# Kernel tuning notes

Hardware: AMD Instinct MI355X
Metric: run time of the kernel (lower is better)

The kernel has to match this reference:

```python
import jax, jax.numpy as jnp
import numpy as np

L = 262144
C = 64           # in_channels == out_channels (required by zeros_like scatter)
NUM_MODES = 64

def setup_inputs() -> dict:
    key = jax.random.key(0)
    k1, k2, k3, k4 = jax.random.split(key, 4)
    u = jax.random.normal(k1, (L, C), dtype=jnp.float32)
    y = jax.random.uniform(k2, (1, 1), dtype=jnp.float32)
    scale = 1.0 / (C * C)
    K = scale * jax.random.normal(k3, (2, C, C, NUM_MODES), dtype=jnp.float32)
    # glorot_normal for square (C, C)
    W = jax.random.normal(k4, (C, C), dtype=jnp.float32) * jnp.sqrt(2.0 / (C + C))
    return {"u": u, "y": y, "K": K, "W": W}

def reference(u, y, K, W):
    num_modes = K.shape[-1]
    out_ch = W.shape[0]
    # conditioner: spectral (global) branch
    u_hat = jnp.fft.rfft(u, axis=0)                      # (L//2+1, C) complex64
    Kc = K[0] + 1j * K[1]                                # (C, C, num_modes)
    z_modes = jnp.einsum('xi,iox->xo', u_hat[:num_modes], Kc)  # (num_modes, C)
    z_global = jnp.zeros_like(u_hat).at[:num_modes, :].set(z_modes)
    # conditioner: local branch (gather one spatial row, apply W)
    length = u.shape[0]
    idx = jnp.int32(y * length)[0][0]
    z_local = jnp.dot(W, u[idx, :out_ch])                # (C,)
    # basefield: inverse transform + local shift
    n = 2 * (z_global.shape[0] - 1)                      # == L
    s = jnp.fft.irfft(z_global, n=n, axis=0)             # (L, C)
    return s + z_local
```

## Files before the change

### kernel.cpp

```cpp
#include <hip/hip_runtime.h>

#define LN 262144
#define LMASK 262143
#define NCH 64
#define INV_L (1.0f/262144.0f)
#define BSTR 38
#define ISTR 138
#define XSTR 66

typedef short short8 __attribute__((ext_vector_type(8)));
typedef float f32x4 __attribute__((ext_vector_type(4)));

static __device__ __forceinline__ unsigned short f2bf(float x) {
    union { float f; unsigned u; } v; v.f = x;
    unsigned r = (v.u + 0x7fff + ((v.u >> 16) & 1)) >> 16;
    return (unsigned short)r;
}
static __device__ __forceinline__ float fsin01(float rev) {
    float r; asm("v_sin_f32 %0, %1" : "=v"(r) : "v"(rev)); return r;
}
static __device__ __forceinline__ float fcos01(float rev) {
    float r; asm("v_cos_f32 %0, %1" : "=v"(r) : "v"(rev)); return r;
}

__global__ __launch_bounds__(256) void fno_fwd(const float* __restrict__ u,
                                               float* __restrict__ part, int nb) {
    __shared__ __align__(16) unsigned short Bt[2][64 * BSTR];
    const int tid = threadIdx.x;
    const int lane = tid & 63;
    const int w = tid >> 6;
    const int chunk = LN / nb;
    const int ksteps = chunk >> 5;
    const int n0 = blockIdx.x * chunk;

    const int kkst = tid >> 3;
    const int gst = tid & 7;

    const int l15 = lane & 15;
    const int hk = lane >> 4;
    const int m = w * 16 + l15;

    float cR[8], sR[8];
    #pragma unroll
    for (int j = 0; j < 8; ++j) {
        int ph = (m * (n0 + hk * 8 + j)) & LMASK;
        cR[j] = fcos01((float)ph * INV_L);
        sR[j] = fsin01((float)ph * INV_L);
    }
    float cD, sD;
    {
        int ph = (m * 32) & LMASK;
        cD = fcos01((float)ph * INV_L);
        sD = fsin01((float)ph * INV_L);
    }

    f32x4 accC[4], accS[4];
    #pragma unroll
    for (int t = 0; t < 4; ++t) { accC[t] = (f32x4){0,0,0,0}; accS[t] = (f32x4){0,0,0,0}; }

    const float* __restrict__ ub = u + (size_t)(n0 + kkst) * NCH + gst * 8;
    const size_t tstep = 32 * NCH;

    float4 a0 = *(const float4*)(ub);
    float4 a1 = *(const float4*)(ub + 4);
    float4 b0 = *(const float4*)(ub + tstep);
    float4 b1 = *(const float4*)(ub + tstep + 4);
    {
        float uv[8] = {a0.x, a0.y, a0.z, a0.w, a1.x, a1.y, a1.z, a1.w};
        #pragma unroll
        for (int q = 0; q < 8; ++q)
            Bt[0][(gst * 8 + q) * BSTR + kkst] = f2bf(uv[q]);
    }
    a0 = b0; a1 = b1;
    b0 = *(const float4*)(ub + 2 * tstep);
    b1 = *(const float4*)(ub + 2 * tstep + 4);

    for (int t = 0; t < ksteps; ++t) {
        __syncthreads();
        if (t + 1 < ksteps) {
            float uv[8] = {a0.x, a0.y, a0.z, a0.w, a1.x, a1.y, a1.z, a1.w};
            unsigned short* bt = Bt[(t + 1) & 1];
            #pragma unroll
            for (int q = 0; q < 8; ++q)
                bt[(gst * 8 + q) * BSTR + kkst] = f2bf(uv[q]);
        }
        a0 = b0; a1 = b1;
        if (t + 3 < ksteps) {
            const float* pn = ub + (size_t)(t + 3) * tstep;
            b0 = *(const float4*)(pn);
            b1 = *(const float4*)(pn + 4);
        }
        short8 aC, aS;
        #pragma unroll
        for (int j = 0; j < 8; ++j) {
            aC[j] = (short)f2bf(cR[j]);
            aS[j] = (short)f2bf(-sR[j]);
        }
        #pragma unroll
        for (int j = 0; j < 8; ++j) {
            float c2 = cR[j] * cD - sR[j] * sD;
            sR[j] = fmaf(sR[j], cD, cR[j] * sD);
            cR[j] = c2;
        }
        const unsigned short* bt = Bt[t & 1];
        #pragma unroll
        for (int tn = 0; tn < 4; ++tn) {
            const short8 bf = *(const short8*)&bt[(tn * 16 + l15) * BSTR + hk * 8];
            accC[tn] = __builtin_amdgcn_mfma_f32_16x16x32_bf16(aC, bf, accC[tn], 0, 0, 0);
            accS[tn] = __builtin_amdgcn_mfma_f32_16x16x32_bf16(aS, bf, accS[tn], 0, 0, 0);
        }
    }
    float* baseR = part + (size_t)blockIdx.x * 8192;
    #pragma unroll
    for (int tn = 0; tn < 4; ++tn) {
        #pragma unroll
        for (int r = 0; r < 4; ++r) {
            int k = w * 16 + hk * 4 + r;
            int i = tn * 16 + l15;
            baseR[k * 64 + i] = accC[tn][r];
            baseR[4096 + k * 64 + i] = accS[tn][r];
        }
    }
}

__global__ __launch_bounds__(512) void fno_redcoef(const float* __restrict__ part, int nb,
                                                   const float* __restrict__ Kt,
                                                   const float* __restrict__ W,
                                                   const float* __restrict__ u,
                                                   const float* __restrict__ y,
                                                   float* __restrict__ coef) {
    const int k = blockIdx.x;
    const int t = threadIdx.x;
    const int j = t & 127;
    const int h = t >> 7;

    const float* __restrict__ pb = part + (size_t)k * 64 + (j & 63) + ((j >> 6) ? 4096 : 0);
    float s = 0.f;
    #pragma unroll 8
    for (int b = h; b < nb; b += 4)
        s += pb[(size_t)b * 8192];

    __shared__ float red[4][128];
    __shared__ float uh[128];
    red[h][j] = s;
    __syncthreads();
    if (t < 128) uh[t] = red[0][t] + red[1][t] + red[2][t] + red[3][t];
    __syncthreads();

    if (t < 64) {
        const int o = t;
        float zr = 0.f, zi = 0.f;
        #pragma unroll 8
        for (int ii = 0; ii < 64; ++ii) {
            float k0v = Kt[(size_t)(ii * 64 + o) * 64 + k];
            float k1v = Kt[262144 + (size_t)(ii * 64 + o) * 64 + k];
            zr = fmaf(uh[ii], k0v, fmaf(-uh[64 + ii], k1v, zr));
            zi = fmaf(uh[ii], k1v, fmaf(uh[64 + ii], k0v, zi));
        }
        if (k == 0) {
            const int idx = (int)(y[0] * (float)LN);
            float zl = 0.f;
            for (int ii = 0; ii < 64; ++ii)
                zl = fmaf(W[o * 64 + ii], u[(size_t)idx * 64 + ii], zl);
            coef[o] = zr * INV_L;
            coef[4096 + o] = 0.f;
            coef[8192 + o] = zl;
        } else {
            coef[k * 64 + o] = 2.f * zr * INV_L;
            coef[4096 + k * 64 + o] = -2.f * zi * INV_L;
        }
    }
}

__global__ __launch_bounds__(256) void fno_inv(const float* __restrict__ coef,
                                               float* __restrict__ out) {
    __shared__ __align__(16) unsigned short Bs[64 * ISTR];
    __shared__ float zloc[64];
    __shared__ float xpose[4][16 * XSTR];
    const int tid = threadIdx.x;
    const int lane = tid & 63;
    const int w = tid >> 6;

    for (int e = tid; e < 4096; e += 256) {
        int mm = e >> 6, ch = e & 63;
        Bs[ch * ISTR + mm] = f2bf(coef[e]);
        Bs[ch * ISTR + 64 + mm] = f2bf(coef[4096 + e]);
    }
    if (tid < 64) zloc[tid] = coef[8192 + tid];
    __syncthreads();

    const int l15 = lane & 15;
    const int hk = lane >> 4;
    const int rl = lane >> 4;
    const int cq = lane & 15;
    float4 zv = *(const float4*)&zloc[cq * 4];

    for (int p = 0; p < 4; ++p) {
        const int nbase = blockIdx.x * 256 + (p * 4 + w) * 16;
        const int row = nbase + l15;
        float cstp = fcos01((float)row * INV_L);
        float sstp = fsin01((float)row * INV_L);

        short8 aF[4];
        #pragma unroll
        for (int h = 0; h < 2; ++h) {
            const int m0 = h * 32 + hk * 8;
            const int ph = (row * m0) & LMASK;
            float c = fcos01((float)ph * INV_L);
            float s = fsin01((float)ph * INV_L);
            #pragma unroll
            for (int jj = 0; jj < 8; ++jj) {
                aF[h][jj] = (short)f2bf(c);
                aF[2 + h][jj] = (short)f2bf(s);
                float c2 = c * cstp - s * sstp;
                s = fmaf(s, cstp, c * sstp);
                c = c2;
            }
        }

        f32x4 acc[4];
        #pragma unroll
        for (int tn = 0; tn < 4; ++tn) acc[tn] = (f32x4){0,0,0,0};
        #pragma unroll
        for (int ks = 0; ks < 4; ++ks) {
            #pragma unroll
            for (int tn = 0; tn < 4; ++tn) {
                const short8 bf = *(const short8*)&Bs[(tn * 16 + l15) * ISTR + ks * 32 + hk * 8];
                acc[tn] = __builtin_amdgcn_mfma_f32_16x16x32_bf16(aF[ks], bf, acc[tn], 0, 0, 0);
            }
        }
        #pragma unroll
        for (int tn = 0; tn < 4; ++tn)
            #pragma unroll
            for (int r = 0; r < 4; ++r)
                xpose[w][(hk * 4 + r) * XSTR + tn * 16 + l15] = acc[tn][r];
        __builtin_amdgcn_s_waitcnt(0);
        #pragma unroll
        for (int rg = 0; rg < 4; ++rg) {
            const int rowl = rg * 4 + rl;
            float4 v = *(const float4*)&xpose[w][rowl * XSTR + cq * 4];
            v.x += zv.x; v.y += zv.y; v.z += zv.z; v.w += zv.w;
            *(float4*)(out + (size_t)(nbase + rowl) * NCH + cq * 4) = v;
        }
    }
}

extern "C" void kernel_launch(void* const* d_in, const int* in_sizes, int n_in,
                              void* d_out, int out_size, void* d_ws, size_t ws_size,
                              hipStream_t stream) {
    const float* u = (const float*)d_in[0];
    const float* y = (const float*)d_in[1];
    const float* K = (const float*)d_in[2];
    const float* W = (const float*)d_in[3];
    float* out = (float*)d_out;
    float* ws = (float*)d_ws;

    int nb = 512;
    while (nb > 64 && ((size_t)(nb * 8192 + 8256) * 4) > ws_size) nb >>= 1;

    float* part = ws;
    float* coef = ws + (size_t)nb * 8192;

    fno_fwd<<<nb, 256, 0, stream>>>(u, part, nb);
    fno_redcoef<<<64, 512, 0, stream>>>(part, nb, K, W, u, y, coef);
    fno_inv<<<1024, 256, 0, stream>>>(coef, out);
}
```

Measured before the change: 64.72 us.

## Split reduction and mode-mixing into separate kernels, raise forward block count

Replaces the fused reduce+coefficient kernel with two kernels. The first reduces the per-block partial DFT sums with contiguous, coalesced reads and computes the local W·u term in an extra block. The second mixes modes through K using coalesced K loads and a transposed shared-memory copy of u_hat. The forward block count doubles to 1024 where workspace allows, which gives more parallelism in fno_fwd but means more partial sums to reduce and adds one more kernel launch. The bf16 conversion now uses the library intrinsic.

```diff
diff --git a/kernel.cpp b/kernel.cpp
--- a/kernel.cpp
+++ b/kernel.cpp
@@ -1,4 +1,5 @@
 #include <hip/hip_runtime.h>
+#include <hip/hip_bf16.h>
 
 #define LN 262144
 #define LMASK 262143
@@ -12,9 +13,9 @@
 typedef float f32x4 __attribute__((ext_vector_type(4)));
 
 static __device__ __forceinline__ unsigned short f2bf(float x) {
-    union { float f; unsigned u; } v; v.f = x;
-    unsigned r = (v.u + 0x7fff + ((v.u >> 16) & 1)) >> 16;
-    return (unsigned short)r;
+    union { __hip_bfloat16 b; unsigned short u; } cv;
+    cv.b = __float2bfloat16(x);
+    return cv.u;
 }
 static __device__ __forceinline__ float fsin01(float rev) {
     float r; asm("v_sin_f32 %0, %1" : "=v"(r) : "v"(rev)); return r;
@@ -123,52 +124,67 @@
     }
 }
 
-__global__ __launch_bounds__(512) void fno_redcoef(const float* __restrict__ part, int nb,
-                                                   const float* __restrict__ Kt,
-                                                   const float* __restrict__ W,
-                                                   const float* __restrict__ u,
-                                                   const float* __restrict__ y,
-                                                   float* __restrict__ coef) {
-    const int k = blockIdx.x;
-    const int t = threadIdx.x;
-    const int j = t & 127;
-    const int h = t >> 7;
-
-    const float* __restrict__ pb = part + (size_t)k * 64 + (j & 63) + ((j >> 6) ? 4096 : 0);
+__global__ __launch_bounds__(256) void fno_red(const float* __restrict__ part, int nb,
+                                               const float* __restrict__ W,
+                                               const float* __restrict__ u,
+                                               const float* __restrict__ y,
+                                               float* __restrict__ uhat,
+                                               float* __restrict__ coef) {
+    const int tid = threadIdx.x;
+    if (blockIdx.x == 64) {
+        if (tid < 64) {
+            const int idx = (int)(y[0] * (float)LN);
+            float zl = 0.f;
+            #pragma unroll 8
+            for (int ii = 0; ii < 64; ++ii)
+                zl = fmaf(W[tid * 64 + ii], u[(size_t)idx * 64 + ii], zl);
+            coef[8192 + tid] = zl;
+        }
+        return;
+    }
+    const int g = blockIdx.x * 128 + (tid & 127);
+    const int h = tid >> 7;
     float s = 0.f;
     #pragma unroll 8
-    for (int b = h; b < nb; b += 4)
-        s += pb[(size_t)b * 8192];
-
-    __shared__ float red[4][128];
-    __shared__ float uh[128];
-    red[h][j] = s;
+    for (int b = h; b < nb; b += 2)
+        s += part[(size_t)b * 8192 + g];
+    __shared__ float sh[2][128];
+    sh[h][tid & 127] = s;
     __syncthreads();
-    if (t < 128) uh[t] = red[0][t] + red[1][t] + red[2][t] + red[3][t];
+    if (h == 0) uhat[g] = sh[0][tid] + sh[1][tid];
+}
+
+__global__ __launch_bounds__(512) void fno_coef(const float* __restrict__ uhat,
+                                                const float* __restrict__ Kt,
+                                                float* __restrict__ coef) {
+    __shared__ float ure[64 * 65], uim[64 * 65];
+    const int tid = threadIdx.x;
+    for (int e = tid; e < 4096; e += 512) {
+        int k = e >> 6, ii = e & 63;
+        ure[ii * 65 + k] = uhat[e];
+        uim[ii * 65 + k] = uhat[4096 + e];
+    }
     __syncthreads();
-
-    if (t < 64) {
-        const int o = t;
-        float zr = 0.f, zi = 0.f;
-        #pragma unroll 8
-        for (int ii = 0; ii < 64; ++ii) {
-            float k0v = Kt[(size_t)(ii * 64 + o) * 64 + k];
-            float k1v = Kt[262144 + (size_t)(ii * 64 + o) * 64 + k];
-            zr = fmaf(uh[ii], k0v, fmaf(-uh[64 + ii], k1v, zr));
-            zi = fmaf(uh[ii], k1v, fmaf(uh[64 + ii], k0v, zi));
-        }
-        if (k == 0) {
-            const int idx = (int)(y[0] * (float)LN);
-            float zl = 0.f;
-            for (int ii = 0; ii < 64; ++ii)
-                zl = fmaf(W[o * 64 + ii], u[(size_t)idx * 64 + ii], zl);
-            coef[o] = zr * INV_L;
-            coef[4096 + o] = 0.f;
-            coef[8192 + o] = zl;
-        } else {
-            coef[k * 64 + o] = 2.f * zr * INV_L;
-            coef[4096 + k * 64 + o] = -2.f * zi * INV_L;
-        }
+    const int m = tid & 63;
+    const int o = blockIdx.x * 8 + (tid >> 6);
+    const float* __restrict__ K0 = Kt + (size_t)o * 64 + m;
+    const float* __restrict__ K1 = K0 + 262144;
+    float zr = 0.f, zi = 0.f;
+    #pragma unroll 8
+    for (int ii = 0; ii < 64; ++ii) {
+        float k0 = K0[(size_t)ii * 4096];
+        float k1 = K1[(size_t)ii * 4096];
+        float re = ure[ii * 65 + m];
+        float im = uim[ii * 65 + m];
+        zr = fmaf(re, k0, fmaf(-im, k1, zr));
+        zi = fmaf(re, k1, fmaf(im, k0, zi));
+    }
+    if (m == 0) {
+        coef[o] = zr * INV_L;
+        coef[4096 + o] = 0.f;
+    } else {
+        coef[m * 64 + o] = 2.f * zr * INV_L;
+        coef[4096 + m * 64 + o] = -2.f * zi * INV_L;
     }
 }
 
@@ -255,13 +271,15 @@
     float* out = (float*)d_out;
     float* ws = (float*)d_ws;
 
-    int nb = 512;
-    while (nb > 64 && ((size_t)(nb * 8192 + 8256) * 4) > ws_size) nb >>= 1;
+    int nb = 1024;
+    while (nb > 64 && ((size_t)(nb * 8192 + 8192 + 8256) * 4) > ws_size) nb >>= 1;
 
     float* part = ws;
-    float* coef = ws + (size_t)nb * 8192;
+    float* uhat = ws + (size_t)nb * 8192;
+    float* coef = uhat + 8192;
 
     fno_fwd<<<nb, 256, 0, stream>>>(u, part, nb);
-    fno_redcoef<<<64, 512, 0, stream>>>(part, nb, K, W, u, y, coef);
+    fno_red<<<65, 256, 0, stream>>>(part, nb, W, u, y, uhat, coef);
+    fno_coef<<<8, 512, 0, stream>>>(uhat, K, coef);
     fno_inv<<<1024, 256, 0, stream>>>(coef, out);
 }
```

Measured after the change: 75.82 us. +17.2%, slower.
